# Kernel optimization log

Measured on AMD Instinct MI355X. Metric: run time of the kernel, lower is better.

The kernel has to match this reference:

```python
import jax, jax.numpy as jnp
import numpy as np

B, S, D = 4, 1024, 1024
H, DK, DH = 16, 64, 64  # num_heads, key_size, head_size
NEG = 1e12


def setup_inputs() -> dict:
    key = jax.random.key(0)
    ks = jax.random.split(key, 16)
    scale = 0.02
    inp = {
        'q': jax.random.normal(ks[0], (B, S, D), jnp.float32),
        'k': jax.random.normal(ks[1], (B, S, D), jnp.float32),
        'v': jax.random.normal(ks[2], (B, S, D), jnp.float32),
        'v_mask': jax.random.randint(ks[3], (B, S), 0, 2, jnp.int32),
        'q_mask': jax.random.randint(ks[4], (B, S), 0, 2, jnp.int32),
        # causal attention mask (float, 1 = keep)
        'a_mask': jnp.tril(jnp.ones((S, S), jnp.float32))[None, None, :, :],
        'Wq': jax.random.normal(ks[5], (D, H * DK), jnp.float32) * scale,
        'bq': jnp.zeros((H * DK,), jnp.float32),
        'Wk': jax.random.normal(ks[6], (D, H * DK), jnp.float32) * scale,
        'bk': jnp.zeros((H * DK,), jnp.float32),
        'Wv': jax.random.normal(ks[7], (D, H * DH), jnp.float32) * scale,
        'bv': jnp.zeros((H * DH,), jnp.float32),
        'Wo': jax.random.normal(ks[8], (H * DH, H * DH), jnp.float32) * scale,
        'bo': jnp.zeros((H * DH,), jnp.float32),
    }
    return inp


def reference(q, k, v, v_mask, q_mask, a_mask, Wq, bq, Wk, bk, Wv, bv, Wo, bo):
    b, sq, _ = q.shape
    sk = k.shape[1]
    qw = (jnp.einsum('bsd,de->bse', q, Wq) + bq).reshape(b, sq, H, DK)
    kw = (jnp.einsum('bsd,de->bse', k, Wk) + bk).reshape(b, sk, H, DK)
    vw = (jnp.einsum('bsd,de->bse', v, Wv) + bv).reshape(b, sk, H, DH)
    # scores [b, h, sq, sk]
    a = jnp.einsum('bjhd,bkhd->bhjk', qw, kw) / jnp.sqrt(jnp.float32(DK))
    vm = v_mask.astype(jnp.float32)  # [b, sk]
    a = a - (1.0 - vm)[:, None, None, :] * NEG  # sequence_masking mode='add'
    a = a - (1.0 - a_mask) * NEG                # attention mask
    p = jax.nn.softmax(a, axis=-1)
    o = jnp.einsum('bhjk,bkhd->bjhd', p, vw).reshape(b, sq, H * DH)
    o = jnp.einsum('bse,ef->bsf', o, Wo) + bo
    qm = q_mask.astype(jnp.float32)
    o = o * qm[:, :, None]  # sequence_masking mode='mul'
    return o
```

## Files before the change

### kernel.cpp

```cpp
#include <hip/hip_runtime.h>
#include <cstdint>
#include <cstddef>

typedef unsigned short u16;
using short8 = __attribute__((ext_vector_type(8))) short;
using f32x4  = __attribute__((ext_vector_type(4))) float;

constexpr int Sc = 1024;
constexpr float PEN = 60.0f;

__device__ __forceinline__ u16 f2bf(float f) {
  union { float f; uint32_t u; } v; v.f = f;
  return (u16)((v.u + 0x7fffu + ((v.u >> 16) & 1u)) >> 16);
}

__device__ __forceinline__ void gload_lds16(const u16* g, u16* l) {
  __builtin_amdgcn_global_load_lds(
      (const __attribute__((address_space(1))) uint32_t*)g,
      (__attribute__((address_space(3))) uint32_t*)l, 16, 0, 0);
}

__device__ __forceinline__ f32x4 mfma16(short8 a, short8 b, f32x4 c) {
  return __builtin_amdgcn_mfma_f32_16x16x32_bf16(a, b, c, 0, 0, 0);
}

__global__ __launch_bounds__(256) void prep(
    const float* __restrict__ q, const float* __restrict__ k,
    const float* __restrict__ v, u16* __restrict__ qb, u16* __restrict__ kb,
    u16* __restrict__ vb, const float* __restrict__ W0,
    const float* __restrict__ W1, const float* __restrict__ W2,
    const float* __restrict__ W3, u16* __restrict__ D0, u16* __restrict__ D1,
    u16* __restrict__ D2, u16* __restrict__ D3) {
  const int y = blockIdx.y;
  if (y < 3) {
    const float* src = y == 0 ? q : y == 1 ? k : v;
    u16* dst = y == 0 ? qb : y == 1 ? kb : vb;
    int i = blockIdx.x * 256 + threadIdx.x;
    float4 a = ((const float4*)src)[2 * i];
    float4 b = ((const float4*)src)[2 * i + 1];
    u16 t[8] = {f2bf(a.x), f2bf(a.y), f2bf(a.z), f2bf(a.w),
                f2bf(b.x), f2bf(b.y), f2bf(b.z), f2bf(b.w)};
    ((uint4*)dst)[i] = *(const uint4*)t;
  } else {
    if (blockIdx.x >= 1024) return;
    const int z = y - 3;
    const float* W = z == 0 ? W0 : z == 1 ? W1 : z == 2 ? W2 : W3;
    u16* WT = z == 0 ? D0 : z == 1 ? D1 : z == 2 ? D2 : D3;
    __shared__ float t[32][33];
    int bx = (blockIdx.x & 31) * 32, by = (blockIdx.x >> 5) * 32;
    int tx = threadIdx.x & 31, ty = threadIdx.x >> 5;
    for (int i = 0; i < 32; i += 8)
      t[ty + i][tx] = W[(size_t)(by + ty + i) * 1024 + bx + tx];
    __syncthreads();
    for (int i = 0; i < 32; i += 8)
      WT[(size_t)(bx + ty + i) * 1024 + by + tx] = f2bf(t[tx][ty + i]);
  }
}

__global__ __launch_bounds__(256, 3) void gemm_qkv(
    const u16* __restrict__ qb, const u16* __restrict__ kb,
    const u16* __restrict__ vb, const u16* __restrict__ BT,
    const float* __restrict__ bq, const float* __restrict__ bk,
    const float* __restrict__ bv, u16* __restrict__ QW, u16* __restrict__ KW,
    u16* __restrict__ VTg) {
  const int bid = blockIdx.x;
  const int xcd = bid & 7, local = bid >> 3;
  const int mp = local & 3, nbi = local >> 2;
  const int m0 = (xcd * 4 + mp) * 128, n0 = nbi * 128;
  const int seg = nbi >> 3;
  const u16* A    = seg == 0 ? qb : seg == 1 ? kb : vb;
  const float* bias = seg == 0 ? bq : seg == 1 ? bk : bv;

  __shared__ u16 As0[128 * 32], As1[128 * 32];
  __shared__ u16 Bs0[128 * 32], Bs1[128 * 32];

  const int t = threadIdx.x, w = t >> 6, lane = t & 63;
  const int q4 = lane >> 4, lm = lane & 15;
  const int wm = (w >> 1) * 64, wn = (w & 1) * 64;
  const int srow = lane >> 2, p = lane & 3;
  const int cf = q4 ^ ((lm >> 2) & 3);

  const int rb0 = (w * 2) * 16, rb1 = (w * 2 + 1) * 16;
  const int row0 = rb0 + srow, row1 = rb1 + srow;
  const int c0 = p ^ ((row0 >> 2) & 3), c1 = p ^ ((row1 >> 2) & 3);
  const u16* pa0 = &A[(size_t)(m0 + row0) * 1024 + c0 * 8];
  const u16* pa1 = &A[(size_t)(m0 + row1) * 1024 + c1 * 8];
  const u16* pb0 = &BT[(size_t)(n0 + row0) * 1024 + c0 * 8];
  const u16* pb1 = &BT[(size_t)(n0 + row1) * 1024 + c1 * 8];

  f32x4 acc[4][4] = {};

  auto stage = [&](u16* as, u16* bs) {
    gload_lds16(pa0, as + rb0 * 32);
    gload_lds16(pa1, as + rb1 * 32);
    gload_lds16(pb0, bs + rb0 * 32);
    gload_lds16(pb1, bs + rb1 * 32);
    pa0 += 32; pa1 += 32; pb0 += 32; pb1 += 32;
  };
  auto compute = [&](const u16* as, const u16* bs) {
    short8 af[4], bf[4];
    for (int mi = 0; mi < 4; ++mi)
      af[mi] = *(const short8*)&as[(wm + mi * 16 + lm) * 32 + cf * 8];
    for (int ni = 0; ni < 4; ++ni)
      bf[ni] = *(const short8*)&bs[(wn + ni * 16 + lm) * 32 + cf * 8];
    for (int mi = 0; mi < 4; ++mi)
      for (int ni = 0; ni < 4; ++ni)
        acc[mi][ni] = mfma16(af[mi], bf[ni], acc[mi][ni]);
  };

  stage(As0, Bs0);
  for (int it = 0; it < 16; ++it) {
    __syncthreads();
    stage(As1, Bs1);
    compute(As0, Bs0);
    __syncthreads();
    if (it < 15) stage(As0, Bs0);
    compute(As1, Bs1);
  }

  if (seg < 2) {
    u16* C = seg == 0 ? QW : KW;
    for (int mi = 0; mi < 4; ++mi)
      for (int ni = 0; ni < 4; ++ni)
        for (int r = 0; r < 4; ++r) {
          int row = m0 + wm + mi * 16 + q4 * 4 + r;
          int col = (n0 + wn + ni * 16 + lm) & 1023;
          C[(size_t)row * 1024 + col] = f2bf(acc[mi][ni][r] + bias[col]);
        }
  } else {
    for (int mi = 0; mi < 4; ++mi)
      for (int ni = 0; ni < 4; ++ni) {
        int row0s = m0 + wm + mi * 16 + q4 * 4;
        int col = (n0 + wn + ni * 16 + lm) & 1023;
        float bv4 = bias[col];
        u16 o4[4];
        for (int r = 0; r < 4; ++r) o4[r] = f2bf(acc[mi][ni][r] + bv4);
        *(uint2*)&VTg[(size_t)col * 4096 + row0s] = *(const uint2*)o4;
      }
  }
}

__global__ __launch_bounds__(256, 4) void gemm_out(
    const u16* __restrict__ A, const u16* __restrict__ BT,
    const float* __restrict__ bias, const int* __restrict__ qmask,
    float* __restrict__ Cf) {
  const int bid = blockIdx.x;
  const int xcd = bid & 7, local = bid >> 3;
  const int mp = local & 7, nb = local >> 3;
  const int m0 = (xcd * 8 + mp) * 64, n0 = nb * 64;

  __shared__ u16 As0[64 * 32], As1[64 * 32];
  __shared__ u16 Bs0[64 * 32], Bs1[64 * 32];
  const int t = threadIdx.x, w = t >> 6, lane = t & 63;
  const int q4 = lane >> 4, lm = lane & 15;
  const int wm = (w >> 1) * 32, wn = (w & 1) * 32;
  const int srow = lane >> 2, p = lane & 3;
  const int cf = q4 ^ ((lm >> 2) & 3);

  const int rb = w * 16;
  const int rowS = rb + srow;
  const int cS = p ^ ((rowS >> 2) & 3);
  const u16* pa = &A[(size_t)(m0 + rowS) * 1024 + cS * 8];
  const u16* pb = &BT[(size_t)(n0 + rowS) * 1024 + cS * 8];

  f32x4 acc[2][2] = {};

  auto stage = [&](u16* as, u16* bs) {
    gload_lds16(pa, as + rb * 32);
    gload_lds16(pb, bs + rb * 32);
    pa += 32; pb += 32;
  };
  auto compute = [&](const u16* as, const u16* bs) {
    short8 af[2], bf[2];
    for (int mi = 0; mi < 2; ++mi)
      af[mi] = *(const short8*)&as[(wm + mi * 16 + lm) * 32 + cf * 8];
    for (int ni = 0; ni < 2; ++ni)
      bf[ni] = *(const short8*)&bs[(wn + ni * 16 + lm) * 32 + cf * 8];
    for (int mi = 0; mi < 2; ++mi)
      for (int ni = 0; ni < 2; ++ni)
        acc[mi][ni] = mfma16(af[mi], bf[ni], acc[mi][ni]);
  };

  stage(As0, Bs0);
  for (int it = 0; it < 16; ++it) {
    __syncthreads();
    stage(As1, Bs1);
    compute(As0, Bs0);
    __syncthreads();
    if (it < 15) stage(As0, Bs0);
    compute(As1, Bs1);
  }

  for (int mi = 0; mi < 2; ++mi)
    for (int ni = 0; ni < 2; ++ni)
      for (int r = 0; r < 4; ++r) {
        int row = m0 + wm + mi * 16 + q4 * 4 + r;
        int col = n0 + wn + ni * 16 + lm;
        Cf[(size_t)row * 1024 + col] =
            (acc[mi][ni][r] + bias[col]) * (float)qmask[row];
      }
}

__global__ __launch_bounds__(64, 3) void attn(
    const u16* __restrict__ QW, const u16* __restrict__ KW,
    const u16* __restrict__ VTg, const int* __restrict__ vmask,
    u16* __restrict__ O) {
  const int bid = blockIdx.x;
  const int X = bid >> 8;
  const int rA = (bid >> 6) & 3, rB = 3 - rA;
  const int bh = bid & 63;
  const int b = bh >> 4, h = bh & 15;
  const int lane = threadIdx.x;
  const int q4 = lane >> 4, lm = lane & 15;

  const int qtA = X, qtB = 15 - X;
  const int TA = 2 * qtA + (rA >> 1), TB = 2 * qtB + (rB >> 1);
  const int RA = qtA * 64 + rA * 16, RB = qtB * 64 + rB * 16;

  __shared__ u16 Ks[2][32 * 64];
  __shared__ float penf[1024];

  {
    const int4* vmp = (const int4*)(vmask + b * 1024);
    for (int j = 0; j < 4; ++j) {
      int4 vm = vmp[4 * lane + j];
      float4 p4;
      p4.x = (1.f - (float)vm.x) * PEN;
      p4.y = (1.f - (float)vm.y) * PEN;
      p4.z = (1.f - (float)vm.z) * PEN;
      p4.w = (1.f - (float)vm.w) * PEN;
      *(float4*)&penf[16 * lane + 4 * j] = p4;
    }
  }
  int anyA = 0, anyB = 0;
  for (int i = lane; i <= qtB * 64; i += 64) {
    int un = (penf[i] == 0.f);
    if (i <= qtA * 64) anyA |= un;
    anyB |= un;
  }
  const int extA = (__ballot(anyA) == 0);
  const int extB = (__ballot(anyB) == 0);
  const int kend = (extA || extB) ? 31 : TB;

  short8 qfA[2], qfB[2];
  auto loadQ = [&](int R, short8 (&qf)[2]) {
    const u16* qp = &QW[(size_t)(b * Sc + R + lm) * 1024 + h * 64];
    qf[0] = *(const short8*)&qp[q4 * 8];
    qf[1] = *(const short8*)&qp[32 + q4 * 8];
    for (int fi = 0; fi < 2; ++fi)
      for (int i = 0; i < 8; ++i) {
        u16 x = (u16)qf[fi][i];
        int e = (x >> 7) & 0xff;
        qf[fi][i] = (short)(e > 3 ? (u16)(x - 0x180) : (u16)(x & 0x8000));
      }
  };
  loadQ(RA, qfA);
  loadQ(RB, qfB);

  float lsA = 0.f, lsB = 0.f;
  f32x4 oaccA[4] = {}, oaccB[4] = {};
  const int qrowA = RA + lm, qrowB = RB + lm;

  const u16* Kbase = &KW[(size_t)(b * Sc) * 1024 + h * 64];
  const u16* Vbase = &VTg[(size_t)(h * 64) * 4096 + b * Sc];

  const int r0 = lane >> 3, pos = lane & 7, ch = pos ^ r0;
  auto stageK = [&](int kt, int buf) {
    for (int j = 0; j < 4; ++j) {
      int lrow = j * 8 + r0;
      int key = 2 * (lrow & 15) + (lrow >> 4);
      gload_lds16(Kbase + (size_t)(kt * 32 + key) * 1024 + ch * 8,
                  &Ks[buf][j * 512]);
    }
  };

  auto strip = [&](const short8 (&qf)[2], f32x4 (&oacc)[4], float& lsum,
                   int Tdiag, int qrow, int kt, int buf, const short8 (&vf)[4]) {
    const int mode = kt > Tdiag ? 2 : (kt == Tdiag ? 1 : 0);
    f32x4 sacc[2] = {};
    __builtin_amdgcn_s_setprio(1);
#pragma unroll
    for (int ni = 0; ni < 2; ++ni) {
      int row = ni * 16 + lm;
      short8 kf0 = *(const short8*)&Ks[buf][row * 64 + ((q4 ^ (lm & 7)) * 8)];
      short8 kf1 = *(const short8*)&Ks[buf][row * 64 + (((4 + q4) ^ (lm & 7)) * 8)];
      sacc[ni] = mfma16(kf0, qf[0], sacc[ni]);
      sacc[ni] = mfma16(kf1, qf[1], sacc[ni]);
    }
    __builtin_amdgcn_s_setprio(0);

    f32x4 pna = *(const f32x4*)&penf[kt * 32 + 8 * q4];
    f32x4 pnb = *(const f32x4*)&penf[kt * 32 + 8 * q4 + 4];
    float pv[2][4];
#pragma unroll
    for (int ni = 0; ni < 2; ++ni)
#pragma unroll
      for (int r = 0; r < 4; ++r) {
        const int j = 2 * r + ni;
        float pen = j < 4 ? pna[j] : pnb[j - 4];
        float x = sacc[ni][r] - pen;
        if (mode == 2) x -= PEN;
        else if (mode == 1) {
          int key = kt * 32 + 8 * q4 + j;
          if (key > qrow) x -= PEN;
        }
        float e = __expf(x);
        lsum += e;
        pv[ni][r] = e;
      }
    uint32_t W0, W1, W2, W3;
    asm("v_cvt_pk_bf16_f32 %0, %1, %2" : "=v"(W0) : "v"(pv[0][0]), "v"(pv[1][0]));
    asm("v_cvt_pk_bf16_f32 %0, %1, %2" : "=v"(W1) : "v"(pv[0][1]), "v"(pv[1][1]));
    asm("v_cvt_pk_bf16_f32 %0, %1, %2" : "=v"(W2) : "v"(pv[0][2]), "v"(pv[1][2]));
    asm("v_cvt_pk_bf16_f32 %0, %1, %2" : "=v"(W3) : "v"(pv[0][3]), "v"(pv[1][3]));
    union { uint32_t u[4]; short8 s; } pk;
    pk.u[0] = W0; pk.u[1] = W1; pk.u[2] = W2; pk.u[3] = W3;
    __builtin_amdgcn_s_setprio(1);
#pragma unroll
    for (int ni = 0; ni < 4; ++ni)
      oacc[ni] = mfma16(pk.s, vf[ni], oacc[ni]);
    __builtin_amdgcn_s_setprio(0);
  };

  stageK(0, 0);
  for (int kt = 0; kt <= kend; ++kt) {
    const int buf = kt & 1;
    short8 vf[4];
#pragma unroll
    for (int ni = 0; ni < 4; ++ni)
      vf[ni] = *(const short8*)(Vbase + (size_t)(ni * 16 + lm) * 4096 +
                                kt * 32 + q4 * 8);
    if (kt < kend) {
      stageK(kt + 1, buf ^ 1);
      asm volatile("s_waitcnt vmcnt(8)" ::: "memory");
    } else {
      asm volatile("s_waitcnt vmcnt(4)" ::: "memory");
    }
    __builtin_amdgcn_sched_barrier(0);

    if (kt <= TA) strip(qfA, oaccA, lsA, TA, qrowA, kt, buf, vf);
    else if (extA) strip(qfA, oaccA, lsA, TA, qrowA, kt, buf, vf);
    if (kt <= TB) strip(qfB, oaccB, lsB, TB, qrowB, kt, buf, vf);
    else if (extB) strip(qfB, oaccB, lsB, TB, qrowB, kt, buf, vf);
  }

  auto epilogue = [&](f32x4 (&oacc)[4], float lsum, int Rbase) {
    float l = lsum;
    l += __shfl_xor(l, 16, 64);
    l += __shfl_xor(l, 32, 64);
    float linv[4];
#pragma unroll
    for (int r = 0; r < 4; ++r) {
      float lr = __shfl(l, (lane & 48) | (q4 * 4 + r), 64);
      linv[r] = 1.0f / lr;
    }
#pragma unroll
    for (int ni = 0; ni < 4; ++ni)
#pragma unroll
      for (int r = 0; r < 4; ++r) {
        int row = b * Sc + Rbase + q4 * 4 + r;
        O[(size_t)row * 1024 + h * 64 + ni * 16 + lm] =
            f2bf(oacc[ni][r] * linv[r]);
      }
  };
  epilogue(oaccA, lsA, RA);
  epilogue(oaccB, lsB, RB);
}

extern "C" void kernel_launch(void* const* d_in, const int* in_sizes, int n_in,
                              void* d_out, int out_size, void* d_ws, size_t ws_size,
                              hipStream_t stream) {
  (void)in_sizes; (void)n_in; (void)out_size; (void)ws_size;
  const float* q  = (const float*)d_in[0];
  const float* k  = (const float*)d_in[1];
  const float* v  = (const float*)d_in[2];
  const int* vmask = (const int*)d_in[3];
  const int* qmask = (const int*)d_in[4];
  const float* Wq = (const float*)d_in[6];
  const float* bq = (const float*)d_in[7];
  const float* Wk = (const float*)d_in[8];
  const float* bk = (const float*)d_in[9];
  const float* Wv = (const float*)d_in[10];
  const float* bv = (const float*)d_in[11];
  const float* Wo = (const float*)d_in[12];
  const float* bo = (const float*)d_in[13];

  char* ws = (char*)d_ws;
  u16* WT3 = (u16*)ws;
  u16* WoT = (u16*)(ws + 6291456);
  u16* QW  = (u16*)(ws + 8388608);
  u16* KW  = (u16*)(ws + 16777216);
  u16* VTg = (u16*)(ws + 25165824);
  u16* Oat = (u16*)(ws + 33554432);
  u16* qb = (u16*)d_out;
  u16* kb = (u16*)d_out + 4194304;
  u16* vb = Oat;

  dim3 tb(256);
  prep<<<dim3(2048, 7), tb, 0, stream>>>(q, k, v, qb, kb, vb, Wq, Wk, Wv, Wo,
                                         WT3, WT3 + 1048576, WT3 + 2097152,
                                         WoT);
  gemm_qkv<<<dim3(768), tb, 0, stream>>>(qb, kb, vb, WT3, bq, bk, bv, QW, KW,
                                         VTg);
  attn<<<dim3(2048), dim3(64), 0, stream>>>(QW, KW, VTg, vmask, Oat);
  gemm_out<<<dim3(1024), tb, 0, stream>>>(Oat, WoT, bo, qmask, (float*)d_out);
}
```

Baseline: 213.7 us.

## Enlarge output GEMM tiles to 128x128 and compact attention mask to bytes

The output projection GEMM moves from 64x64 to 128x128 tiles, with each wave computing a 64x64 sub-tile of 4x4 MFMAs and the grid shrinking from 1024 to 256 blocks. This is meant to raise data reuse per LDS load and cut global traffic. The cost is fewer blocks (256 on a 256-CU part), higher register use, and a lower occupancy hint. In attention, the value-mask penalty table shrinks from floats to bytes and is decoded once per key tile for both strips, and the launch-bounds occupancy hint rises from 3 to 4.

```diff
diff --git a/kernel.cpp b/kernel.cpp
--- a/kernel.cpp
+++ b/kernel.cpp
@@ -140,44 +140,49 @@
   }
 }
 
-__global__ __launch_bounds__(256, 4) void gemm_out(
+__global__ __launch_bounds__(256, 3) void gemm_out(
     const u16* __restrict__ A, const u16* __restrict__ BT,
     const float* __restrict__ bias, const int* __restrict__ qmask,
     float* __restrict__ Cf) {
   const int bid = blockIdx.x;
   const int xcd = bid & 7, local = bid >> 3;
-  const int mp = local & 7, nb = local >> 3;
-  const int m0 = (xcd * 8 + mp) * 64, n0 = nb * 64;
-
-  __shared__ u16 As0[64 * 32], As1[64 * 32];
-  __shared__ u16 Bs0[64 * 32], Bs1[64 * 32];
+  const int mp = local & 3, nb = local >> 2;
+  const int m0 = (xcd * 4 + mp) * 128, n0 = nb * 128;
+
+  __shared__ u16 As0[128 * 32], As1[128 * 32];
+  __shared__ u16 Bs0[128 * 32], Bs1[128 * 32];
+
   const int t = threadIdx.x, w = t >> 6, lane = t & 63;
   const int q4 = lane >> 4, lm = lane & 15;
-  const int wm = (w >> 1) * 32, wn = (w & 1) * 32;
+  const int wm = (w >> 1) * 64, wn = (w & 1) * 64;
   const int srow = lane >> 2, p = lane & 3;
   const int cf = q4 ^ ((lm >> 2) & 3);
 
-  const int rb = w * 16;
-  const int rowS = rb + srow;
-  const int cS = p ^ ((rowS >> 2) & 3);
-  const u16* pa = &A[(size_t)(m0 + rowS) * 1024 + cS * 8];
-  const u16* pb = &BT[(size_t)(n0 + rowS) * 1024 + cS * 8];
-
-  f32x4 acc[2][2] = {};
+  const int rb0 = (w * 2) * 16, rb1 = (w * 2 + 1) * 16;
+  const int row0 = rb0 + srow, row1 = rb1 + srow;
+  const int c0 = p ^ ((row0 >> 2) & 3), c1 = p ^ ((row1 >> 2) & 3);
+  const u16* pa0 = &A[(size_t)(m0 + row0) * 1024 + c0 * 8];
+  const u16* pa1 = &A[(size_t)(m0 + row1) * 1024 + c1 * 8];
+  const u16* pb0 = &BT[(size_t)(n0 + row0) * 1024 + c0 * 8];
+  const u16* pb1 = &BT[(size_t)(n0 + row1) * 1024 + c1 * 8];
+
+  f32x4 acc[4][4] = {};
 
   auto stage = [&](u16* as, u16* bs) {
-    gload_lds16(pa, as + rb * 32);
-    gload_lds16(pb, bs + rb * 32);
-    pa += 32; pb += 32;
+    gload_lds16(pa0, as + rb0 * 32);
+    gload_lds16(pa1, as + rb1 * 32);
+    gload_lds16(pb0, bs + rb0 * 32);
+    gload_lds16(pb1, bs + rb1 * 32);
+    pa0 += 32; pa1 += 32; pb0 += 32; pb1 += 32;
   };
   auto compute = [&](const u16* as, const u16* bs) {
-    short8 af[2], bf[2];
-    for (int mi = 0; mi < 2; ++mi)
+    short8 af[4], bf[4];
+    for (int mi = 0; mi < 4; ++mi)
       af[mi] = *(const short8*)&as[(wm + mi * 16 + lm) * 32 + cf * 8];
-    for (int ni = 0; ni < 2; ++ni)
+    for (int ni = 0; ni < 4; ++ni)
       bf[ni] = *(const short8*)&bs[(wn + ni * 16 + lm) * 32 + cf * 8];
-    for (int mi = 0; mi < 2; ++mi)
-      for (int ni = 0; ni < 2; ++ni)
+    for (int mi = 0; mi < 4; ++mi)
+      for (int ni = 0; ni < 4; ++ni)
         acc[mi][ni] = mfma16(af[mi], bf[ni], acc[mi][ni]);
   };
 
@@ -191,8 +196,8 @@
     compute(As1, Bs1);
   }
 
-  for (int mi = 0; mi < 2; ++mi)
-    for (int ni = 0; ni < 2; ++ni)
+  for (int mi = 0; mi < 4; ++mi)
+    for (int ni = 0; ni < 4; ++ni)
       for (int r = 0; r < 4; ++r) {
         int row = m0 + wm + mi * 16 + q4 * 4 + r;
         int col = n0 + wn + ni * 16 + lm;
@@ -201,7 +206,7 @@
       }
 }
 
-__global__ __launch_bounds__(64, 3) void attn(
+__global__ __launch_bounds__(64, 4) void attn(
     const u16* __restrict__ QW, const u16* __restrict__ KW,
     const u16* __restrict__ VTg, const int* __restrict__ vmask,
     u16* __restrict__ O) {
@@ -218,23 +223,21 @@
   const int RA = qtA * 64 + rA * 16, RB = qtB * 64 + rB * 16;
 
   __shared__ u16 Ks[2][32 * 64];
-  __shared__ float penf[1024];
+  __shared__ unsigned char penb[1024];
 
   {
     const int4* vmp = (const int4*)(vmask + b * 1024);
     for (int j = 0; j < 4; ++j) {
       int4 vm = vmp[4 * lane + j];
-      float4 p4;
-      p4.x = (1.f - (float)vm.x) * PEN;
-      p4.y = (1.f - (float)vm.y) * PEN;
-      p4.z = (1.f - (float)vm.z) * PEN;
-      p4.w = (1.f - (float)vm.w) * PEN;
-      *(float4*)&penf[16 * lane + 4 * j] = p4;
+      unsigned char m4[4] = {
+          (unsigned char)(vm.x == 0), (unsigned char)(vm.y == 0),
+          (unsigned char)(vm.z == 0), (unsigned char)(vm.w == 0)};
+      *(unsigned int*)&penb[16 * lane + 4 * j] = *(const unsigned int*)m4;
     }
   }
   int anyA = 0, anyB = 0;
   for (int i = lane; i <= qtB * 64; i += 64) {
-    int un = (penf[i] == 0.f);
+    int un = (penb[i] == 0);
     if (i <= qtA * 64) anyA |= un;
     anyB |= un;
   }
@@ -275,7 +278,8 @@
   };
 
   auto strip = [&](const short8 (&qf)[2], f32x4 (&oacc)[4], float& lsum,
-                   int Tdiag, int qrow, int kt, int buf, const short8 (&vf)[4]) {
+                   int Tdiag, int qrow, int kt, int buf, const short8 (&vf)[4],
+                   const float (&pen8)[8]) {
     const int mode = kt > Tdiag ? 2 : (kt == Tdiag ? 1 : 0);
     f32x4 sacc[2] = {};
     __builtin_amdgcn_s_setprio(1);
@@ -289,16 +293,13 @@
     }
     __builtin_amdgcn_s_setprio(0);
 
-    f32x4 pna = *(const f32x4*)&penf[kt * 32 + 8 * q4];
-    f32x4 pnb = *(const f32x4*)&penf[kt * 32 + 8 * q4 + 4];
     float pv[2][4];
 #pragma unroll
     for (int ni = 0; ni < 2; ++ni)
 #pragma unroll
       for (int r = 0; r < 4; ++r) {
         const int j = 2 * r + ni;
-        float pen = j < 4 ? pna[j] : pnb[j - 4];
-        float x = sacc[ni][r] - pen;
+        float x = sacc[ni][r] - pen8[j];
         if (mode == 2) x -= PEN;
         else if (mode == 1) {
           int key = kt * 32 + 8 * q4 + j;
@@ -338,10 +339,18 @@
     }
     __builtin_amdgcn_sched_barrier(0);
 
-    if (kt <= TA) strip(qfA, oaccA, lsA, TA, qrowA, kt, buf, vf);
-    else if (extA) strip(qfA, oaccA, lsA, TA, qrowA, kt, buf, vf);
-    if (kt <= TB) strip(qfB, oaccB, lsB, TB, qrowB, kt, buf, vf);
-    else if (extB) strip(qfB, oaccB, lsB, TB, qrowB, kt, buf, vf);
+    uint2 pw = *(const uint2*)&penb[kt * 32 + 8 * q4];
+    float pen8[8];
+#pragma unroll
+    for (int j = 0; j < 8; ++j) {
+      uint32_t wv = j < 4 ? pw.x : pw.y;
+      pen8[j] = ((wv >> (8 * (j & 3))) & 1u) ? PEN : 0.f;
+    }
+
+    if (kt <= TA) strip(qfA, oaccA, lsA, TA, qrowA, kt, buf, vf, pen8);
+    else if (extA) strip(qfA, oaccA, lsA, TA, qrowA, kt, buf, vf, pen8);
+    if (kt <= TB) strip(qfB, oaccB, lsB, TB, qrowB, kt, buf, vf, pen8);
+    else if (extB) strip(qfB, oaccB, lsB, TB, qrowB, kt, buf, vf, pen8);
   }
 
   auto epilogue = [&](f32x4 (&oacc)[4], float lsum, int Rbase) {
@@ -403,5 +412,5 @@
   gemm_qkv<<<dim3(768), tb, 0, stream>>>(qb, kb, vb, WT3, bq, bk, bv, QW, KW,
                                          VTg);
   attn<<<dim3(2048), dim3(64), 0, stream>>>(QW, KW, VTg, vmask, Oat);
-  gemm_out<<<dim3(1024), tb, 0, stream>>>(Oat, WoT, bo, qmask, (float*)d_out);
-}
+  gemm_out<<<dim3(256), tb, 0, stream>>>(Oat, WoT, bo, qmask, (float*)d_out);
+}
```

New measurement: 219.4 us. 2.7% more time.
